# Optimization experiments

Measured on AMD Instinct MI355X. Metric: run time of the kernel, lower is better.

## Reference

```python
import jax, jax.numpy as jnp
import numpy as np

VEC_DIM = 128
NUM_DOCS = 1_000_000
NUM_WORDS = 100_000
BATCH = 16_384
K = 26  # num_noise_words + 1


def setup_inputs() -> dict:
    key = jax.random.key(0)
    k1, k2, k3, k4 = jax.random.split(key, 4)
    return {
        "context_ids": jax.random.randint(k1, (BATCH,), 0, NUM_WORDS, dtype=jnp.int32),
        "doc_ids": jax.random.randint(k2, (BATCH,), 0, NUM_DOCS, dtype=jnp.int32),
        "target_noise_ids": jax.random.randint(k3, (BATCH, K), 0, NUM_WORDS, dtype=jnp.int32),
        # learned parameters
        "D": jax.random.normal(k4, (NUM_DOCS, VEC_DIM), dtype=jnp.float32),
        "O": jnp.zeros((VEC_DIM, NUM_WORDS), dtype=jnp.float32),
    }


def reference(context_ids, doc_ids, target_noise_ids, D, O):
    # context_ids is unused in the original forward.
    d = D[doc_ids]                 # [B, V]  gather doc vectors
    w = O.T[target_noise_ids]      # [B, K, V] gather word (output) vectors
    # scores: batched dot products, equivalent to bmm(d[:,None,:], w.transpose) then squeeze
    return jnp.einsum("bv,bkv->bk", d, w)
```

## Files before the change

### kernel.cpp

```cpp
#include <hip/hip_runtime.h>

#define BATCH   16384
#define KK      26
#define VDIM    128
#define NWORDS  100000

template <int CTRL>
__device__ __forceinline__ float dpp_mov(float x) {
    int xi = __builtin_bit_cast(int, x);
    int yi = __builtin_amdgcn_update_dpp(0, xi, CTRL, 0xF, 0xF, true);
    return __builtin_bit_cast(float, yi);
}

__global__ __launch_bounds__(256) void transpose_O(const float* __restrict__ O,
                                                   float* __restrict__ Ot) {
    __shared__ float tile[32][129];
    const int wbase = blockIdx.x * 32;
    const int t = threadIdx.x;

    #pragma unroll
    for (int i = 0; i < 4; ++i) {
        int idx = i * 256 + t;
        int v = idx >> 3;
        int w4 = (idx & 7) * 4;
        float4 r = *(const float4*)&O[(size_t)v * NWORDS + wbase + w4];
        tile[w4 + 0][v] = r.x;
        tile[w4 + 1][v] = r.y;
        tile[w4 + 2][v] = r.z;
        tile[w4 + 3][v] = r.w;
    }
    __syncthreads();

    #pragma unroll
    for (int i = 0; i < 4; ++i) {
        int idx = i * 256 + t;
        int w = idx >> 5;
        int v = (idx & 31) * 4;
        *(float4*)&Ot[(size_t)(wbase + w) * VDIM + v] =
            *(const float4*)&tile[w][v];
    }
}

__global__ __launch_bounds__(256) void gather_dot(const int* __restrict__ doc_ids,
                                                  const int* __restrict__ tn_ids,
                                                  const float* __restrict__ D,
                                                  const float* __restrict__ Ot,
                                                  float* __restrict__ out) {
    const int b0 = blockIdx.x * 2;
    const int t = threadIdx.x;
    const int g = t >> 5;
    const int l = t & 31;

    const int doc0 = doc_ids[b0];
    const int doc1 = doc_ids[b0 + 1];
    const float4 dv0 = *(const float4*)&D[(size_t)doc0 * VDIM + l * 4];
    const float4 dv1 = *(const float4*)&D[(size_t)doc1 * VDIM + l * 4];

    int word[2][4];
    #pragma unroll
    for (int j = 0; j < 4; ++j) {
        const int k = g + 8 * j;
        const bool ok = (k < KK);
        word[0][j] = ok ? tn_ids[b0 * KK + k] : 0;
        word[1][j] = ok ? tn_ids[(b0 + 1) * KK + k] : 0;
    }

    float4 wv[2][4];
    #pragma unroll
    for (int m = 0; m < 2; ++m)
        #pragma unroll
        for (int j = 0; j < 4; ++j)
            wv[m][j] = *(const float4*)&Ot[(size_t)word[m][j] * VDIM + l * 4];

    #pragma unroll
    for (int m = 0; m < 2; ++m) {
        const float4 dv = m ? dv1 : dv0;
        const int base = (b0 + m) * KK;
        #pragma unroll
        for (int j = 0; j < 4; ++j) {
            const int k = g + 8 * j;
            float p = dv.x * wv[m][j].x + dv.y * wv[m][j].y
                    + dv.z * wv[m][j].z + dv.w * wv[m][j].w;
            p += dpp_mov<0x111>(p);
            p += dpp_mov<0x112>(p);
            p += dpp_mov<0x114>(p);
            p += dpp_mov<0x118>(p);
            p += dpp_mov<0x142>(p);
            if (l == 31 && k < KK) out[base + k] = p;
        }
    }
}

__global__ __launch_bounds__(256) void gather_dot_direct(const int* __restrict__ doc_ids,
                                                         const int* __restrict__ tn_ids,
                                                         const float* __restrict__ D,
                                                         const float* __restrict__ O,
                                                         float* __restrict__ out) {
    __shared__ float d_s[VDIM];
    const int b = blockIdx.x;

    if (threadIdx.x < VDIM) {
        const int doc = doc_ids[b];
        d_s[threadIdx.x] = D[(size_t)doc * VDIM + threadIdx.x];
    }
    __syncthreads();

    const int wave = threadIdx.x >> 6;
    const int lane = threadIdx.x & 63;
    const int v0 = lane * 2;
    const float2 dv = *(const float2*)&d_s[v0];

    for (int k = wave; k < KK; k += 4) {
        const int word = tn_ids[b * KK + k];
        float p = dv.x * O[(size_t)v0 * NWORDS + word]
                + dv.y * O[(size_t)(v0 + 1) * NWORDS + word];
        #pragma unroll
        for (int off = 32; off > 0; off >>= 1)
            p += __shfl_down(p, off);
        if (lane == 0) out[b * KK + k] = p;
    }
}

extern "C" void kernel_launch(void* const* d_in, const int* in_sizes, int n_in,
                              void* d_out, int out_size, void* d_ws, size_t ws_size,
                              hipStream_t stream) {
    const int*   doc_ids = (const int*)d_in[1];
    const int*   tn_ids  = (const int*)d_in[2];
    const float* D       = (const float*)d_in[3];
    const float* O       = (const float*)d_in[4];
    float*       out     = (float*)d_out;

    const size_t ot_bytes = (size_t)NWORDS * VDIM * sizeof(float);

    if (ws_size >= ot_bytes) {
        float* Ot = (float*)d_ws;
        transpose_O<<<NWORDS / 32, 256, 0, stream>>>(O, Ot);
        gather_dot<<<BATCH / 2, 256, 0, stream>>>(doc_ids, tn_ids, D, Ot, out);
    } else {
        gather_dot_direct<<<BATCH, 256, 0, stream>>>(doc_ids, tn_ids, D, O, out);
    }
}
```

Measured before the change: 612.0 us.

## Pre-gather doc vectors into compact buffer during transpose kernel

The first 2048 blocks of the transpose kernel now also gather the doc vectors for the batch into a contiguous workspace buffer, overlapping that gather with the O transpose. The dot-product kernel then reads those vectors contiguously instead of doing a dependent index load plus a random gather from the 512MB D table. This costs an extra write and read of 8MB and raises the workspace requirement. If the workspace is too small the code falls back to the slow direct kernel.

```diff
diff --git a/kernel.cpp b/kernel.cpp
--- a/kernel.cpp
+++ b/kernel.cpp
@@ -13,10 +13,23 @@
 }
 
 __global__ __launch_bounds__(256) void transpose_O(const float* __restrict__ O,
-                                                   float* __restrict__ Ot) {
+                                                   const int* __restrict__ doc_ids,
+                                                   const float* __restrict__ D,
+                                                   float* __restrict__ Ot,
+                                                   float* __restrict__ Dc) {
     __shared__ float tile[32][129];
     const int wbase = blockIdx.x * 32;
     const int t = threadIdx.x;
+    const int g = t >> 5;
+    const int l = t & 31;
+
+    const int  b_dc   = blockIdx.x * 8 + g;
+    const bool has_dc = (blockIdx.x < BATCH / 8);
+    float4 dreg;
+    if (has_dc) {
+        const int doc = doc_ids[b_dc];
+        dreg = *(const float4*)&D[(size_t)doc * VDIM + l * 4];
+    }
 
     #pragma unroll
     for (int i = 0; i < 4; ++i) {
@@ -39,11 +52,13 @@
         *(float4*)&Ot[(size_t)(wbase + w) * VDIM + v] =
             *(const float4*)&tile[w][v];
     }
+
+    if (has_dc)
+        *(float4*)&Dc[(size_t)b_dc * VDIM + l * 4] = dreg;
 }
 
-__global__ __launch_bounds__(256) void gather_dot(const int* __restrict__ doc_ids,
-                                                  const int* __restrict__ tn_ids,
-                                                  const float* __restrict__ D,
+__global__ __launch_bounds__(256) void gather_dot(const int* __restrict__ tn_ids,
+                                                  const float* __restrict__ Dc,
                                                   const float* __restrict__ Ot,
                                                   float* __restrict__ out) {
     const int b0 = blockIdx.x * 2;
@@ -51,10 +66,8 @@
     const int g = t >> 5;
     const int l = t & 31;
 
-    const int doc0 = doc_ids[b0];
-    const int doc1 = doc_ids[b0 + 1];
-    const float4 dv0 = *(const float4*)&D[(size_t)doc0 * VDIM + l * 4];
-    const float4 dv1 = *(const float4*)&D[(size_t)doc1 * VDIM + l * 4];
+    const float4 dv0 = *(const float4*)&Dc[(size_t)b0 * VDIM + l * 4];
+    const float4 dv1 = *(const float4*)&Dc[(size_t)(b0 + 1) * VDIM + l * 4];
 
     int word[2][4];
     #pragma unroll
@@ -131,11 +144,13 @@
     float*       out     = (float*)d_out;
 
     const size_t ot_bytes = (size_t)NWORDS * VDIM * sizeof(float);
+    const size_t dc_bytes = (size_t)BATCH * VDIM * sizeof(float);
 
-    if (ws_size >= ot_bytes) {
+    if (ws_size >= ot_bytes + dc_bytes) {
         float* Ot = (float*)d_ws;
-        transpose_O<<<NWORDS / 32, 256, 0, stream>>>(O, Ot);
-        gather_dot<<<BATCH / 2, 256, 0, stream>>>(doc_ids, tn_ids, D, Ot, out);
+        float* Dc = (float*)((char*)d_ws + ot_bytes);
+        transpose_O<<<NWORDS / 32, 256, 0, stream>>>(O, doc_ids, D, Ot, Dc);
+        gather_dot<<<BATCH / 2, 256, 0, stream>>>(tn_ids, Dc, Ot, out);
     } else {
         gather_dot_direct<<<BATCH, 256, 0, stream>>>(doc_ids, tn_ids, D, O, out);
     }
```

Measured after the change: 615.9 us. No clear change (+0.6%).
